# Optimization experiments

Hardware: AMD Instinct MI355X
Metric: run time of the kernel (lower is better)

Reference implementation:

```python
import jax, jax.numpy as jnp
import numpy as np


def conv2d(x, w, pad=1):
    return jax.lax.conv_general_dilated(
        x, w, (1, 1), [(pad, pad), (pad, pad)],
        dimension_numbers=('NCHW', 'OIHW', 'NCHW'))


def bn(x, g, b, m, v, eps=1e-5):
    inv = g / jnp.sqrt(v + eps)
    return x * inv[None, :, None, None] + (b - m * inv)[None, :, None, None]


def deform_conv(x, wp, bp, wd):
    # v2-style DeformConv2D: internal p_conv -> offsets, bilinear sample, 3x3 conv
    b, c, h, w = x.shape
    ks = 3
    N = ks * ks
    offset = conv2d(x, wp, 1) + bp[None, :, None, None]   # (b, 2N, h, w)
    xp = jnp.pad(x, ((0, 0), (0, 0), (1, 1), (1, 1)))     # zero_padding(1)
    Hp, Wp = h + 2, w + 2
    off = offset.transpose(0, 2, 3, 1)                    # (b, h, w, 2N)
    pn_y, pn_x = jnp.meshgrid(jnp.arange(-1, 2), jnp.arange(-1, 2), indexing='ij')
    # sampling locations p = p_0 + p_n + offset (in padded coords)
    py = jnp.arange(1, h + 1)[None, :, None, None] + pn_y.reshape(-1)[None, None, None, :] + off[..., :N]
    px = jnp.arange(1, w + 1)[None, None, :, None] + pn_x.reshape(-1)[None, None, None, :] + off[..., N:]
    fy = jnp.floor(jax.lax.stop_gradient(py))
    fx = jnp.floor(jax.lax.stop_gradient(px))
    qy0 = jnp.clip(fy, 0, Hp - 1); qy1 = jnp.clip(fy + 1, 0, Hp - 1)
    qx0 = jnp.clip(fx, 0, Wp - 1); qx1 = jnp.clip(fx + 1, 0, Wp - 1)
    py = jnp.clip(py, 0, Hp - 1); px = jnp.clip(px, 0, Wp - 1)
    g_lt = (1 + (qy0 - py)) * (1 + (qx0 - px))
    g_rb = (1 - (qy1 - py)) * (1 - (qx1 - px))
    g_lb = (1 + (qy0 - py)) * (1 - (qx1 - px))
    g_rt = (1 - (qy1 - py)) * (1 + (qx0 - px))
    flat = xp.reshape(b, c, Hp * Wp)

    def gather(qy, qx):
        idx = (qy * Wp + qx).astype(jnp.int32).reshape(b, 1, -1)
        return jnp.take_along_axis(flat, idx, axis=2).reshape(b, c, h, w, N)

    x_off = (g_lt[:, None] * gather(qy0, qx0) + g_rb[:, None] * gather(qy1, qx1)
             + g_lb[:, None] * gather(qy0, qx1) + g_rt[:, None] * gather(qy1, qx0))
    outc = wd.shape[0]
    # equivalent to _reshape_x_offset + Conv2d(kernel=ks, stride=ks)
    return jnp.einsum('bchwn,ocn->bohw', x_off, wd.reshape(outc, c, N))


def setup_inputs() -> dict:
    key = jax.random.key(0)
    ks = jax.random.split(key, 24)
    B, H, W = 256, 28, 28

    def nrm(k, s, sc=1.0):
        return jax.random.normal(k, s, jnp.float32) * sc

    return {
        'x': nrm(ks[0], (B, 3, H, W)),
        'w1': nrm(ks[1], (32, 3, 3, 3), 0.2),
        'g1': jax.random.uniform(ks[2], (32,), jnp.float32) + 0.5,
        'b1': nrm(ks[3], (32,), 0.1),
        'm1': nrm(ks[4], (32,), 0.1),
        'v1': jax.random.uniform(ks[5], (32,), jnp.float32) + 0.5,
        'wp': nrm(ks[6], (18, 32, 3, 3), 0.01),  # p_conv: small offsets
        'bp': nrm(ks[7], (18,), 0.1),
        'w2': nrm(ks[8], (32, 32, 3, 3), 0.1),
        'g2': jax.random.uniform(ks[9], (32,), jnp.float32) + 0.5,
        'b2': nrm(ks[10], (32,), 0.1),
        'm2': nrm(ks[11], (32,), 0.1),
        'v2': jax.random.uniform(ks[12], (32,), jnp.float32) + 0.5,
        'w3': nrm(ks[13], (64, 32, 3, 3), 0.1),
        'g3': jax.random.uniform(ks[14], (64,), jnp.float32) + 0.5,
        'b3': nrm(ks[15], (64,), 0.1),
        'm3': nrm(ks[16], (64,), 0.1),
        'v3': jax.random.uniform(ks[17], (64,), jnp.float32) + 0.5,
        'wc': nrm(ks[18], (10, 64), 0.1),
        'bc': nrm(ks[19], (10,), 0.1),
    }


def reference(x, w1, g1, b1, m1, v1, wp, bp, w2, g2, b2, m2, v2,
              w3, g3, b3, m3, v3, wc, bc):
    h = bn(jax.nn.relu(conv2d(x, w1)), g1, b1, m1, v1)
    h = bn(jax.nn.relu(deform_conv(h, wp, bp, w2)), g2, b2, m2, v2)
    h = bn(jax.nn.relu(conv2d(h, w3)), g3, b3, m3, v3)
    h = h.mean(axis=(2, 3))               # avg_pool2d(28) on 28x28 -> global mean
    logits = h @ wc.T + bc
    return jax.nn.log_softmax(logits, axis=1)
```

## Files before the change

kernel.cpp:

```cpp
#include <hip/hip_runtime.h>
#include <hip/hip_bf16.h>
#include <math.h>

typedef __attribute__((ext_vector_type(8))) short short8;
typedef __attribute__((ext_vector_type(4))) float floatx4;
typedef __attribute__((ext_vector_type(2))) float floatx2;

#define NB  256

#define WPBF_OFF  0u
#define W2BF_OFF  18432u
#define W3BF_OFF  36864u
#define POOL_OFF  73728u
#define C1P_OFF   139264u
#define C3P_OFF   139520u
#define W1BF_OFF  140032u

#define L_IMG1  0
#define L_U     50240
#define L_OFFT  100480
#define L_WL    114304
#define L_TOT   152192

static __device__ __forceinline__ unsigned short f2bf(float f) {
    unsigned u = __float_as_uint(f);
    u = (u + 0x7fffu + ((u >> 16) & 1u)) >> 16;
    return (unsigned short)u;
}

static __device__ __forceinline__ unsigned pk2bf(float a, float b) {
    __hip_bfloat162 h = __float22bfloat162_rn(make_float2(a, b));
    unsigned r;
    __builtin_memcpy(&r, &h, 4);
    return r;
}

static __device__ __forceinline__ floatx2 up2(unsigned u) {
    floatx2 r;
    r.x = __uint_as_float(u << 16);
    r.y = __uint_as_float(u & 0xffff0000u);
    return r;
}

__global__ void wcvt(const float* __restrict__ wp, const float* __restrict__ w2,
                     const float* __restrict__ w3, const float* __restrict__ w1,
                     const float* __restrict__ g1, const float* __restrict__ b1,
                     const float* __restrict__ m1, const float* __restrict__ v1,
                     const float* __restrict__ g3, const float* __restrict__ b3,
                     const float* __restrict__ m3, const float* __restrict__ v3,
                     unsigned short* __restrict__ wpbf, unsigned short* __restrict__ w2bf,
                     unsigned short* __restrict__ w3bf, unsigned short* __restrict__ w1bf,
                     float* __restrict__ c1p, float* __restrict__ c3p)
{
    int t = blockIdx.x * 256 + threadIdx.x;
    if (t < 9216) {
        int oc = t / 288, k = t % 288;
        int n = k >> 5, ic = k & 31;
        wpbf[t] = (oc < 18) ? f2bf(wp[oc * 288 + ic * 9 + n]) : (unsigned short)0;
    } else if (t < 18432) {
        int i = t - 9216;
        int oc = i / 288, k = i % 288;
        int n = k >> 5, ic = k & 31;
        w2bf[i] = f2bf(w2[oc * 288 + ic * 9 + n]);
    } else if (t < 36864) {
        int i = t - 18432;
        int oc = i / 288, k = i % 288;
        int n = k >> 5, ic = k & 31;
        w3bf[i] = f2bf(w3[oc * 288 + ic * 9 + n]);
    } else if (t < 36928) {
        int oc = t - 36864;
        int c = oc & 31;
        float inv = g1[c] * rsqrtf(v1[c] + 1e-5f);
        c1p[oc] = (oc < 32) ? inv : (b1[c] - m1[c] * inv);
    } else if (t < 37056) {
        int i = t - 36928;
        int k = i & 63;
        float inv = g3[k] * rsqrtf(v3[k] + 1e-5f);
        c3p[i] = (i < 64) ? inv : (b3[k] - m3[k] * inv);
    } else if (t < 38080) {
        int i = t - 37056;
        int oc = i >> 5, k = i & 31;
        int n = k / 3, ic = k - n * 3;
        w1bf[i] = (k < 27) ? f2bf(w1[oc * 27 + ic * 9 + n]) : (unsigned short)0;
    }
}

__global__ __launch_bounds__(768, 3) void fused_all(
    const float* __restrict__ x, const unsigned short* __restrict__ w1bf,
    const float* __restrict__ c1p,
    const unsigned short* __restrict__ wpbf, const float* __restrict__ bp,
    const unsigned short* __restrict__ w2bf,
    const float* __restrict__ g2, const float* __restrict__ b2,
    const float* __restrict__ m2, const float* __restrict__ v2,
    const unsigned short* __restrict__ w3bf,
    float* __restrict__ pooled)
{
    __shared__ __align__(16) unsigned char ALL[L_TOT];
    int t = threadIdx.x, b = blockIdx.x;
    int w = t >> 6, l = t & 63, col = l & 15, q = l >> 4;

    unsigned char* img1 = ALL + L_IMG1;
    unsigned char* uimg = ALL + L_U;
    float* xs = (float*)uimg;

    {
        const float4* xg = (const float4*)(x + (size_t)b * 2352);
        float4* xl = (float4*)uimg;
        for (int i = t; i < 588; i += 768) xl[i] = xg[i];
    }
    {
        const uint4* src = (const uint4*)wpbf;
        for (int i = t; i < 1152; i += 768) {
            int row = i / 36, g = i - row * 36;
            *(uint4*)(ALL + L_WL + row * 592 + g * 16) = src[i];
        }
    }
    if (t == 700) xs[2352] = 0.f;
    if (t < 4)  *(uint4*)(img1 + 784 * 64 + t * 16) = make_uint4(0u, 0u, 0u, 0u);
    if (t >= 4 && t < 8) *(uint4*)(uimg + 784 * 64 + (t - 4) * 16) = make_uint4(0u, 0u, 0u, 0u);

    short8 b2f[18];
#pragma unroll
    for (int n = 0; n < 9; n++) {
        b2f[n]     = *(const short8*)(w2bf + col * 288 + n * 32 + q * 8);
        b2f[9 + n] = *(const short8*)(w2bf + (16 + col) * 288 + n * 32 + q * 8);
    }
    float bias0 = bp[col];
    float bias1 = (col < 2) ? bp[16 + col] : 0.f;
    float inv0 = g2[col] * rsqrtf(v2[col] + 1e-5f);
    float sh0 = b2[col] - m2[col] * inv0;
    float inv1 = g2[16 + col] * rsqrtf(v2[16 + col] + 1e-5f);
    float sh1 = b2[16 + col] - m2[16 + col] * inv1;

    __syncthreads();

    {
        short8 bf0 = *(const short8*)(w1bf + col * 32 + q * 8);
        short8 bf1 = *(const short8*)(w1bf + (16 + col) * 32 + q * 8);
        float sc0 = c1p[col],      s0 = c1p[32 + col];
        float sc1 = c1p[16 + col], s1 = c1p[48 + col];
        for (int mt = w; mt < 49; mt += 12) {
            int p = mt * 16 + col;
            int y = p / 28, xx = p % 28;
            unsigned au[4];
#pragma unroll
            for (int jp = 0; jp < 4; jp++) {
                float vv[2];
#pragma unroll
                for (int h = 0; h < 2; h++) {
                    int k = q * 8 + jp * 2 + h;
                    int n = k / 3, ic = k - n * 3;
                    int yy = y + n / 3 - 1, xc = xx + n % 3 - 1;
                    bool ok = (k < 27) && ((unsigned)yy < 28u) && ((unsigned)xc < 28u);
                    int idx = ok ? (ic * 784 + yy * 28 + xc) : 2352;
                    vv[h] = xs[idx];
                }
                au[jp] = pk2bf(vv[0], vv[1]);
            }
            uint4 a4 = make_uint4(au[0], au[1], au[2], au[3]);
            short8 a = *(short8*)&a4;
            floatx4 d0 = {0.f, 0.f, 0.f, 0.f}, d1 = {0.f, 0.f, 0.f, 0.f};
            d0 = __builtin_amdgcn_mfma_f32_16x16x32_bf16(a, bf0, d0, 0, 0, 0);
            d1 = __builtin_amdgcn_mfma_f32_16x16x32_bf16(a, bf1, d1, 0, 0, 0);
#pragma unroll
            for (int r = 0; r < 4; r++) {
                int pout = mt * 16 + q * 4 + r;
                *(unsigned short*)(img1 + pout * 64 + col * 2) =
                    f2bf(fmaxf(d0[r], 0.f) * sc0 + s0);
                *(unsigned short*)(img1 + pout * 64 + 32 + col * 2) =
                    f2bf(fmaxf(d1[r], 0.f) * sc1 + s1);
            }
        }
    }
    __syncthreads();

    {
        const unsigned char* ib = img1;
        float* otw = (float*)(ALL + L_OFFT) + w * 288;

        for (int mt = w; mt < 49; mt += 12) {
            int p = mt * 16 + col;
            int y = p / 28, xx = p % 28;

            floatx4 a0 = {0.f, 0.f, 0.f, 0.f}, a1 = {0.f, 0.f, 0.f, 0.f};
#pragma unroll
            for (int n = 0; n < 9; n++) {
                int yy = y + n / 3 - 1, xc = xx + n % 3 - 1;
                bool ok = ((unsigned)yy < 28u) && ((unsigned)xc < 28u);
                int tp = ok ? (yy * 28 + xc) : 784;
                short8 a  = *(const short8*)(ib + tp * 64 + q * 16);
                short8 p0 = *(const short8*)(ALL + L_WL + col * 592 + n * 64 + q * 16);
                short8 p1 = *(const short8*)(ALL + L_WL + (16 + col) * 592 + n * 64 + q * 16);
                a0 = __builtin_amdgcn_mfma_f32_16x16x32_bf16(a, p0, a0, 0, 0, 0);
                a1 = __builtin_amdgcn_mfma_f32_16x16x32_bf16(a, p1, a1, 0, 0, 0);
            }
#pragma unroll
            for (int r = 0; r < 4; r++)
                otw[(q * 4 + r) * 18 + col] = a0[r] + bias0;
            if (col < 2) {
#pragma unroll
                for (int r = 0; r < 4; r++)
                    otw[(q * 4 + r) * 18 + 16 + col] = a1[r] + bias1;
            }
            __asm__ volatile("s_waitcnt lgkmcnt(0)" ::: "memory");

            floatx4 d0 = {0.f, 0.f, 0.f, 0.f}, d1 = {0.f, 0.f, 0.f, 0.f};
#pragma unroll
            for (int n = 0; n < 9; n++) {
                float offy = otw[col * 18 + n];
                float offx = otw[col * 18 + 9 + n];
                float py = (float)(y + n / 3) + offy;
                float px = (float)(xx + n % 3) + offx;
                float fy = floorf(py), fx = floorf(px);
                float qy0 = fminf(fmaxf(fy, 0.f), 29.f);
                float qy1 = fminf(fmaxf(fy + 1.f, 0.f), 29.f);
                float qx0 = fminf(fmaxf(fx, 0.f), 29.f);
                float qx1 = fminf(fmaxf(fx + 1.f, 0.f), 29.f);
                float pyc = fminf(fmaxf(py, 0.f), 29.f);
                float pxc = fminf(fmaxf(px, 0.f), 29.f);
                float glt = (1.f + (qy0 - pyc)) * (1.f + (qx0 - pxc));
                float grb = (1.f - (qy1 - pyc)) * (1.f - (qx1 - pxc));
                float glb = (1.f + (qy0 - pyc)) * (1.f - (qx1 - pxc));
                float grt = (1.f - (qy1 - pyc)) * (1.f + (qx0 - pxc));
                int iy0 = (int)qy0, iy1 = (int)qy1, ix0 = (int)qx0, ix1 = (int)qx1;
                int ly0 = iy0 - 1, ly1 = iy1 - 1, lx0 = ix0 - 1, lx1 = ix1 - 1;
                bool v00 = ((unsigned)ly0 < 28u) && ((unsigned)lx0 < 28u);
                bool v11 = ((unsigned)ly1 < 28u) && ((unsigned)lx1 < 28u);
                bool v01 = ((unsigned)ly0 < 28u) && ((unsigned)lx1 < 28u);
                bool v10 = ((unsigned)ly1 < 28u) && ((unsigned)lx0 < 28u);
                int p00 = v00 ? (ly0 * 28 + lx0) : 784;
                int p11 = v11 ? (ly1 * 28 + lx1) : 784;
                int p01 = v01 ? (ly0 * 28 + lx1) : 784;
                int p10 = v10 ? (ly1 * 28 + lx0) : 784;
                uint4 u00 = *(const uint4*)(ib + p00 * 64 + q * 16);
                uint4 u11 = *(const uint4*)(ib + p11 * 64 + q * 16);
                uint4 u01 = *(const uint4*)(ib + p01 * 64 + q * 16);
                uint4 u10 = *(const uint4*)(ib + p10 * 64 + q * 16);
                floatx2 f0 = up2(u00.x) * glt + up2(u11.x) * grb + up2(u01.x) * glb + up2(u10.x) * grt;
                floatx2 f1 = up2(u00.y) * glt + up2(u11.y) * grb + up2(u01.y) * glb + up2(u10.y) * grt;
                floatx2 f2 = up2(u00.z) * glt + up2(u11.z) * grb + up2(u01.z) * glb + up2(u10.z) * grt;
                floatx2 f3 = up2(u00.w) * glt + up2(u11.w) * grb + up2(u01.w) * glb + up2(u10.w) * grt;
                uint4 af4 = make_uint4(pk2bf(f0.x, f0.y), pk2bf(f1.x, f1.y),
                                       pk2bf(f2.x, f2.y), pk2bf(f3.x, f3.y));
                short8 af = *(short8*)&af4;
                d0 = __builtin_amdgcn_mfma_f32_16x16x32_bf16(af, b2f[n], d0, 0, 0, 0);
                d1 = __builtin_amdgcn_mfma_f32_16x16x32_bf16(af, b2f[9 + n], d1, 0, 0, 0);
            }
#pragma unroll
            for (int r = 0; r < 4; r++) {
                int pout = mt * 16 + q * 4 + r;
                *(unsigned short*)(uimg + pout * 64 + col * 2) =
                    f2bf(fmaxf(d0[r], 0.f) * inv0 + sh0);
                *(unsigned short*)(uimg + pout * 64 + 32 + col * 2) =
                    f2bf(fmaxf(d1[r], 0.f) * inv1 + sh1);
            }
        }
    }
    __syncthreads();

    {
        const uint4* src = (const uint4*)w3bf;
        for (int i = t; i < 2304; i += 768) {
            int row = i / 36, g = i - row * 36;
            *(uint4*)(ALL + L_WL + row * 592 + g * 16) = src[i];
        }
    }
    __syncthreads();

    {
        float* part = (float*)(ALL + L_OFFT);
        int ocp = w & 1;
        const unsigned char* ib = uimg;
        float psA = 0.f, psB = 0.f;
        for (int mt = (w >> 1); mt < 49; mt += 6) {
            int p = mt * 16 + col;
            int y = p / 28, xx = p % 28;
            floatx4 cA = {0.f, 0.f, 0.f, 0.f}, cB = {0.f, 0.f, 0.f, 0.f};
#pragma unroll
            for (int n = 0; n < 9; n++) {
                int yy = y + n / 3 - 1, xc = xx + n % 3 - 1;
                bool ok = ((unsigned)yy < 28u) && ((unsigned)xc < 28u);
                int tp = ok ? (yy * 28 + xc) : 784;
                short8 a  = *(const short8*)(ib + tp * 64 + q * 16);
                short8 wA = *(const short8*)(ALL + L_WL + (ocp * 32 + col) * 592 + n * 64 + q * 16);
                short8 wB = *(const short8*)(ALL + L_WL + (ocp * 32 + 16 + col) * 592 + n * 64 + q * 16);
                cA = __builtin_amdgcn_mfma_f32_16x16x32_bf16(a, wA, cA, 0, 0, 0);
                cB = __builtin_amdgcn_mfma_f32_16x16x32_bf16(a, wB, cB, 0, 0, 0);
            }
            psA += fmaxf(cA[0], 0.f) + fmaxf(cA[1], 0.f) + fmaxf(cA[2], 0.f) + fmaxf(cA[3], 0.f);
            psB += fmaxf(cB[0], 0.f) + fmaxf(cB[1], 0.f) + fmaxf(cB[2], 0.f) + fmaxf(cB[3], 0.f);
        }
        psA += __shfl_xor(psA, 16, 64); psA += __shfl_xor(psA, 32, 64);
        psB += __shfl_xor(psB, 16, 64); psB += __shfl_xor(psB, 32, 64);
        if (l < 16) { part[w * 32 + l] = psA; part[w * 32 + 16 + l] = psB; }
        __syncthreads();
        if (t < 64) {
            int hi = t >> 5, c = t & 31;
            float s = 0.f;
#pragma unroll
            for (int j = 0; j < 6; j++) s += part[(2 * j + hi) * 32 + c];
            pooled[(size_t)b * 64 + t] = s;
        }
    }
}

__global__ __launch_bounds__(64) void cls_kernel(
    const float* __restrict__ pooled, const float* __restrict__ c3p,
    const float* __restrict__ wc, const float* __restrict__ bc,
    float* __restrict__ outp)
{
    int b = blockIdx.x * 64 + threadIdx.x;
    float feat[64];
#pragma unroll
    for (int k = 0; k < 64; k++)
        feat[k] = pooled[(size_t)b * 64 + k] * c3p[k] * (1.f / 784.f) + c3p[64 + k];
    float lg[10];
    float mx = -1e30f;
#pragma unroll
    for (int j = 0; j < 10; j++) {
        float s = bc[j];
#pragma unroll
        for (int k = 0; k < 64; k++) s += feat[k] * wc[j * 64 + k];
        lg[j] = s;
        mx = fmaxf(mx, s);
    }
    float se = 0.f;
#pragma unroll
    for (int j = 0; j < 10; j++) se += expf(lg[j] - mx);
    float lse = logf(se);
#pragma unroll
    for (int j = 0; j < 10; j++) outp[b * 10 + j] = lg[j] - mx - lse;
}

extern "C" void kernel_launch(void* const* d_in, const int* in_sizes, int n_in,
                              void* d_out, int out_size, void* d_ws, size_t ws_size,
                              hipStream_t stream)
{
    (void)in_sizes; (void)n_in; (void)out_size; (void)ws_size;
    const float* x  = (const float*)d_in[0];
    const float* w1 = (const float*)d_in[1];
    const float* g1 = (const float*)d_in[2];
    const float* b1 = (const float*)d_in[3];
    const float* m1 = (const float*)d_in[4];
    const float* v1 = (const float*)d_in[5];
    const float* wp = (const float*)d_in[6];
    const float* bp = (const float*)d_in[7];
    const float* w2 = (const float*)d_in[8];
    const float* g2 = (const float*)d_in[9];
    const float* b2 = (const float*)d_in[10];
    const float* m2 = (const float*)d_in[11];
    const float* v2 = (const float*)d_in[12];
    const float* w3 = (const float*)d_in[13];
    const float* g3 = (const float*)d_in[14];
    const float* b3 = (const float*)d_in[15];
    const float* m3 = (const float*)d_in[16];
    const float* v3 = (const float*)d_in[17];
    const float* wc = (const float*)d_in[18];
    const float* bc = (const float*)d_in[19];
    float* outp = (float*)d_out;

    unsigned char* ws = (unsigned char*)d_ws;
    unsigned short* wpbf = (unsigned short*)(ws + WPBF_OFF);
    unsigned short* w2bf = (unsigned short*)(ws + W2BF_OFF);
    unsigned short* w3bf = (unsigned short*)(ws + W3BF_OFF);
    float*          pooled = (float*)(ws + POOL_OFF);
    float*          c1p  = (float*)(ws + C1P_OFF);
    float*          c3p  = (float*)(ws + C3P_OFF);
    unsigned short* w1bf = (unsigned short*)(ws + W1BF_OFF);

    wcvt<<<149, 256, 0, stream>>>(wp, w2, w3, w1, g1, b1, m1, v1, g3, b3, m3, v3,
                                  wpbf, w2bf, w3bf, w1bf, c1p, c3p);
    fused_all<<<NB, 768, 0, stream>>>(x, w1bf, c1p, wpbf, bp, w2bf,
                                      g2, b2, m2, v2, w3bf, pooled);
    cls_kernel<<<4, 64, 0, stream>>>(pooled, c3p, wc, bc, outp);
}
```

Measured before the change: 146.3 us.

## Fuse weight conversion and classifier into a single megakernel launch

Removes the separate weight-conversion and classifier kernels. Each block now converts fp32 weights to bf16 straight into shared memory, computes the BN constants inline, and runs the pooled-feature classifier with log-softmax using wave shuffles. The w2 weights are read from LDS per MFMA instead of being kept in registers. This saves two launches and the global round trips, but every block now redoes the weight conversion with scalar strided global loads, and the inner loop gains extra LDS reads.

```diff
diff --git a/kernel.cpp b/kernel.cpp
--- a/kernel.cpp
+++ b/kernel.cpp
@@ -6,21 +6,13 @@
 typedef __attribute__((ext_vector_type(4))) float floatx4;
 typedef __attribute__((ext_vector_type(2))) float floatx2;
 
-#define NB  256
-
-#define WPBF_OFF  0u
-#define W2BF_OFF  18432u
-#define W3BF_OFF  36864u
-#define POOL_OFF  73728u
-#define C1P_OFF   139264u
-#define C3P_OFF   139520u
-#define W1BF_OFF  140032u
-
-#define L_IMG1  0
-#define L_U     50240
-#define L_OFFT  100480
-#define L_WL    114304
-#define L_TOT   152192
+#define NB 256
+
+#define L_IMG1 0
+#define L_U    50240
+#define L_OFFT 100480
+#define L_WL   114304
+#define L_TOT  152192
 
 static __device__ __forceinline__ unsigned short f2bf(float f) {
     unsigned u = __float_as_uint(f);
@@ -42,58 +34,19 @@
     return r;
 }
 
-__global__ void wcvt(const float* __restrict__ wp, const float* __restrict__ w2,
-                     const float* __restrict__ w3, const float* __restrict__ w1,
-                     const float* __restrict__ g1, const float* __restrict__ b1,
-                     const float* __restrict__ m1, const float* __restrict__ v1,
-                     const float* __restrict__ g3, const float* __restrict__ b3,
-                     const float* __restrict__ m3, const float* __restrict__ v3,
-                     unsigned short* __restrict__ wpbf, unsigned short* __restrict__ w2bf,
-                     unsigned short* __restrict__ w3bf, unsigned short* __restrict__ w1bf,
-                     float* __restrict__ c1p, float* __restrict__ c3p)
-{
-    int t = blockIdx.x * 256 + threadIdx.x;
-    if (t < 9216) {
-        int oc = t / 288, k = t % 288;
-        int n = k >> 5, ic = k & 31;
-        wpbf[t] = (oc < 18) ? f2bf(wp[oc * 288 + ic * 9 + n]) : (unsigned short)0;
-    } else if (t < 18432) {
-        int i = t - 9216;
-        int oc = i / 288, k = i % 288;
-        int n = k >> 5, ic = k & 31;
-        w2bf[i] = f2bf(w2[oc * 288 + ic * 9 + n]);
-    } else if (t < 36864) {
-        int i = t - 18432;
-        int oc = i / 288, k = i % 288;
-        int n = k >> 5, ic = k & 31;
-        w3bf[i] = f2bf(w3[oc * 288 + ic * 9 + n]);
-    } else if (t < 36928) {
-        int oc = t - 36864;
-        int c = oc & 31;
-        float inv = g1[c] * rsqrtf(v1[c] + 1e-5f);
-        c1p[oc] = (oc < 32) ? inv : (b1[c] - m1[c] * inv);
-    } else if (t < 37056) {
-        int i = t - 36928;
-        int k = i & 63;
-        float inv = g3[k] * rsqrtf(v3[k] + 1e-5f);
-        c3p[i] = (i < 64) ? inv : (b3[k] - m3[k] * inv);
-    } else if (t < 38080) {
-        int i = t - 37056;
-        int oc = i >> 5, k = i & 31;
-        int n = k / 3, ic = k - n * 3;
-        w1bf[i] = (k < 27) ? f2bf(w1[oc * 27 + ic * 9 + n]) : (unsigned short)0;
-    }
-}
-
-__global__ __launch_bounds__(768, 3) void fused_all(
-    const float* __restrict__ x, const unsigned short* __restrict__ w1bf,
-    const float* __restrict__ c1p,
-    const unsigned short* __restrict__ wpbf, const float* __restrict__ bp,
-    const unsigned short* __restrict__ w2bf,
+__global__ __launch_bounds__(768, 3) void meganet(
+    const float* __restrict__ x,  const float* __restrict__ w1,
+    const float* __restrict__ g1, const float* __restrict__ b1,
+    const float* __restrict__ m1, const float* __restrict__ v1,
+    const float* __restrict__ wp, const float* __restrict__ bp,
+    const float* __restrict__ w2,
     const float* __restrict__ g2, const float* __restrict__ b2,
     const float* __restrict__ m2, const float* __restrict__ v2,
-    const unsigned short* __restrict__ w3bf,
-    float* __restrict__ pooled)
+    const float* __restrict__ w3,
+    const float* __restrict__ g3, const float* __restrict__ b3,
+    const float* __restrict__ m3, const float* __restrict__ v3,
+    const float* __restrict__ wc, const float* __restrict__ bc,
+    float* __restrict__ outp)
 {
     __shared__ __align__(16) unsigned char ALL[L_TOT];
     int t = threadIdx.x, b = blockIdx.x;
@@ -101,30 +54,33 @@
 
     unsigned char* img1 = ALL + L_IMG1;
     unsigned char* uimg = ALL + L_U;
-    float* xs = (float*)uimg;
 
     {
         const float4* xg = (const float4*)(x + (size_t)b * 2352);
         float4* xl = (float4*)uimg;
         for (int i = t; i < 588; i += 768) xl[i] = xg[i];
     }
-    {
-        const uint4* src = (const uint4*)wpbf;
-        for (int i = t; i < 1152; i += 768) {
-            int row = i / 36, g = i - row * 36;
-            *(uint4*)(ALL + L_WL + row * 592 + g * 16) = src[i];
-        }
-    }
-    if (t == 700) xs[2352] = 0.f;
+    for (int i = t; i < 9216; i += 768) {
+        int row = i / 288, k = i - row * 288;
+        int src = row * 288 + (k & 31) * 9 + (k >> 5);
+        float vp = (row < 18) ? wp[src] : 0.f;
+        *(unsigned short*)(ALL + L_WL + row * 592 + k * 2) = f2bf(vp);
+        *(unsigned short*)(ALL + L_WL + (32 + row) * 592 + k * 2) = f2bf(w2[src]);
+    }
+    for (int i = t; i < 1024; i += 768) {
+        int oc = i >> 5, k = i & 31;
+        int n = k / 3, ic = k - n * 3;
+        float v = (k < 27) ? w1[oc * 27 + ic * 9 + n] : 0.f;
+        *(unsigned short*)(ALL + L_OFFT + i * 2) = f2bf(v);
+    }
+    if (t == 700) ((float*)uimg)[2352] = 0.f;
     if (t < 4)  *(uint4*)(img1 + 784 * 64 + t * 16) = make_uint4(0u, 0u, 0u, 0u);
     if (t >= 4 && t < 8) *(uint4*)(uimg + 784 * 64 + (t - 4) * 16) = make_uint4(0u, 0u, 0u, 0u);
 
-    short8 b2f[18];
-#pragma unroll
-    for (int n = 0; n < 9; n++) {
-        b2f[n]     = *(const short8*)(w2bf + col * 288 + n * 32 + q * 8);
-        b2f[9 + n] = *(const short8*)(w2bf + (16 + col) * 288 + n * 32 + q * 8);
-    }
+    float i1a = g1[col] * rsqrtf(v1[col] + 1e-5f);
+    float sc0 = i1a, s0 = b1[col] - m1[col] * i1a;
+    float i1b = g1[16 + col] * rsqrtf(v1[16 + col] + 1e-5f);
+    float sc1 = i1b, s1 = b1[16 + col] - m1[16 + col] * i1b;
     float bias0 = bp[col];
     float bias1 = (col < 2) ? bp[16 + col] : 0.f;
     float inv0 = g2[col] * rsqrtf(v2[col] + 1e-5f);
@@ -135,10 +91,9 @@
     __syncthreads();
 
     {
-        short8 bf0 = *(const short8*)(w1bf + col * 32 + q * 8);
-        short8 bf1 = *(const short8*)(w1bf + (16 + col) * 32 + q * 8);
-        float sc0 = c1p[col],      s0 = c1p[32 + col];
-        float sc1 = c1p[16 + col], s1 = c1p[48 + col];
+        short8 bf0 = *(const short8*)(ALL + L_OFFT + col * 64 + q * 16);
+        short8 bf1 = *(const short8*)(ALL + L_OFFT + (16 + col) * 64 + q * 16);
+        const float* xs = (const float*)uimg;
         for (int mt = w; mt < 49; mt += 12) {
             int p = mt * 16 + col;
             int y = p / 28, xx = p % 28;
@@ -243,8 +198,10 @@
                 uint4 af4 = make_uint4(pk2bf(f0.x, f0.y), pk2bf(f1.x, f1.y),
                                        pk2bf(f2.x, f2.y), pk2bf(f3.x, f3.y));
                 short8 af = *(short8*)&af4;
-                d0 = __builtin_amdgcn_mfma_f32_16x16x32_bf16(af, b2f[n], d0, 0, 0, 0);
-                d1 = __builtin_amdgcn_mfma_f32_16x16x32_bf16(af, b2f[9 + n], d1, 0, 0, 0);
+                short8 wb0 = *(const short8*)(ALL + L_WL + (32 + col) * 592 + n * 64 + q * 16);
+                short8 wb1 = *(const short8*)(ALL + L_WL + (48 + col) * 592 + n * 64 + q * 16);
+                d0 = __builtin_amdgcn_mfma_f32_16x16x32_bf16(af, wb0, d0, 0, 0, 0);
+                d1 = __builtin_amdgcn_mfma_f32_16x16x32_bf16(af, wb1, d1, 0, 0, 0);
             }
 #pragma unroll
             for (int r = 0; r < 4; r++) {
@@ -258,12 +215,10 @@
     }
     __syncthreads();
 
-    {
-        const uint4* src = (const uint4*)w3bf;
-        for (int i = t; i < 2304; i += 768) {
-            int row = i / 36, g = i - row * 36;
-            *(uint4*)(ALL + L_WL + row * 592 + g * 16) = src[i];
-        }
+    for (int i = t; i < 18432; i += 768) {
+        int row = i / 288, k = i - row * 288;
+        *(unsigned short*)(ALL + L_WL + row * 592 + k * 2) =
+            f2bf(w3[row * 288 + (k & 31) * 9 + (k >> 5)]);
     }
     __syncthreads();
 
@@ -293,50 +248,43 @@
         psA += __shfl_xor(psA, 16, 64); psA += __shfl_xor(psA, 32, 64);
         psB += __shfl_xor(psB, 16, 64); psB += __shfl_xor(psB, 32, 64);
         if (l < 16) { part[w * 32 + l] = psA; part[w * 32 + 16 + l] = psB; }
-        __syncthreads();
-        if (t < 64) {
-            int hi = t >> 5, c = t & 31;
-            float s = 0.f;
-#pragma unroll
-            for (int j = 0; j < 6; j++) s += part[(2 * j + hi) * 32 + c];
-            pooled[(size_t)b * 64 + t] = s;
+    }
+    __syncthreads();
+
+    if (t < 64) {
+        const float* part = (const float*)(ALL + L_OFFT);
+        int hi = t >> 5, c = t & 31;
+        float s = 0.f;
+#pragma unroll
+        for (int j = 0; j < 6; j++) s += part[(2 * j + hi) * 32 + c];
+        float inv3 = g3[t] * rsqrtf(v3[t] + 1e-5f);
+        float feat = s * inv3 * (1.f / 784.f) + (b3[t] - m3[t] * inv3);
+        float lg[10];
+        float mx = -1e30f;
+#pragma unroll
+        for (int j = 0; j < 10; j++) {
+            float v = feat * wc[j * 64 + t];
+            v += __shfl_xor(v, 1, 64);  v += __shfl_xor(v, 2, 64);
+            v += __shfl_xor(v, 4, 64);  v += __shfl_xor(v, 8, 64);
+            v += __shfl_xor(v, 16, 64); v += __shfl_xor(v, 32, 64);
+            lg[j] = v + bc[j];
+            mx = fmaxf(mx, lg[j]);
         }
-    }
-}
-
-__global__ __launch_bounds__(64) void cls_kernel(
-    const float* __restrict__ pooled, const float* __restrict__ c3p,
-    const float* __restrict__ wc, const float* __restrict__ bc,
-    float* __restrict__ outp)
-{
-    int b = blockIdx.x * 64 + threadIdx.x;
-    float feat[64];
-#pragma unroll
-    for (int k = 0; k < 64; k++)
-        feat[k] = pooled[(size_t)b * 64 + k] * c3p[k] * (1.f / 784.f) + c3p[64 + k];
-    float lg[10];
-    float mx = -1e30f;
-#pragma unroll
-    for (int j = 0; j < 10; j++) {
-        float s = bc[j];
-#pragma unroll
-        for (int k = 0; k < 64; k++) s += feat[k] * wc[j * 64 + k];
-        lg[j] = s;
-        mx = fmaxf(mx, s);
-    }
-    float se = 0.f;
-#pragma unroll
-    for (int j = 0; j < 10; j++) se += expf(lg[j] - mx);
-    float lse = logf(se);
-#pragma unroll
-    for (int j = 0; j < 10; j++) outp[b * 10 + j] = lg[j] - mx - lse;
+        float se = 0.f;
+#pragma unroll
+        for (int j = 0; j < 10; j++) se += expf(lg[j] - mx);
+        float lse = logf(se);
+#pragma unroll
+        for (int j = 0; j < 10; j++)
+            if (t == j) outp[(size_t)b * 10 + j] = lg[j] - mx - lse;
+    }
 }
 
 extern "C" void kernel_launch(void* const* d_in, const int* in_sizes, int n_in,
                               void* d_out, int out_size, void* d_ws, size_t ws_size,
                               hipStream_t stream)
 {
-    (void)in_sizes; (void)n_in; (void)out_size; (void)ws_size;
+    (void)in_sizes; (void)n_in; (void)out_size; (void)d_ws; (void)ws_size;
     const float* x  = (const float*)d_in[0];
     const float* w1 = (const float*)d_in[1];
     const float* g1 = (const float*)d_in[2];
@@ -359,18 +307,7 @@
     const float* bc = (const float*)d_in[19];
     float* outp = (float*)d_out;
 
-    unsigned char* ws = (unsigned char*)d_ws;
-    unsigned short* wpbf = (unsigned short*)(ws + WPBF_OFF);
-    unsigned short* w2bf = (unsigned short*)(ws + W2BF_OFF);
-    unsigned short* w3bf = (unsigned short*)(ws + W3BF_OFF);
-    float*          pooled = (float*)(ws + POOL_OFF);
-    float*          c1p  = (float*)(ws + C1P_OFF);
-    float*          c3p  = (float*)(ws + C3P_OFF);
-    unsigned short* w1bf = (unsigned short*)(ws + W1BF_OFF);
-
-    wcvt<<<149, 256, 0, stream>>>(wp, w2, w3, w1, g1, b1, m1, v1, g3, b3, m3, v3,
-                                  wpbf, w2bf, w3bf, w1bf, c1p, c3p);
-    fused_all<<<NB, 768, 0, stream>>>(x, w1bf, c1p, wpbf, bp, w2bf,
-                                      g2, b2, m2, v2, w3bf, pooled);
-    cls_kernel<<<4, 64, 0, stream>>>(pooled, c3p, wc, bc, outp);
-}
+    meganet<<<NB, 768, 0, stream>>>(x, w1, g1, b1, m1, v1, wp, bp, w2,
+                                    g2, b2, m2, v2, w3, g3, b3, m3, v3,
+                                    wc, bc, outp);
+}
```

Result: no change. 143.8 us (-1.7%).
